# Kernel tuning notes

Measured on AMD Instinct MI355X. Metric: run time of the kernel, lower is better.

## Reference

```python
import jax, jax.numpy as jnp
import numpy as np

# structural constants (from dg config / init_kwargs)
B = 8192      # batch (L=1)
N = 64        # number of columns
C = 16        # one-hot width per column
D = N * C     # 1024
NUM = 32      # first NUM columns are numeric (use info['range'])
NCAUSAL = 16  # causal_cols = range(16)
K = 8         # info['range'][i] is [C, K]
HS = 1024
HP = 1024
TAU = 0.7
SMOOTH = 0.1  # kwargs['smoothing']


def setup_inputs() -> dict:
    key = jax.random.key(0)
    ks = jax.random.split(key, 20)
    s = 0.02
    inp = {
        'x': jax.random.uniform(ks[0], (B, D), dtype=jnp.float32),
        'truth_x': jax.random.normal(ks[1], (B, N), dtype=jnp.float32),
        # selector: Linear(D,HS) -> ReLU -> Linear(HS,N) -> Sigmoid
        'sel_w1': jax.random.normal(ks[2], (D, HS)) * s,
        'sel_b1': jnp.zeros((HS,), jnp.float32),
        'sel_w2': jax.random.normal(ks[3], (HS, N)) * s,
        'sel_b2': jnp.zeros((N,), jnp.float32),
        # perturber: D->HP->HP->HP->D with ReLU between
        'pw1': jax.random.normal(ks[4], (D, HP)) * s,
        'pb1': jnp.zeros((HP,), jnp.float32),
        'pw2': jax.random.normal(ks[5], (HP, HP)) * s,
        'pb2': jnp.zeros((HP,), jnp.float32),
        'pw3': jax.random.normal(ks[6], (HP, HP)) * s,
        'pb3': jnp.zeros((HP,), jnp.float32),
        'pw4': jax.random.normal(ks[7], (HP, D)) * s,
        'pb4': jnp.zeros((D,), jnp.float32),
        # dg.info['range'][i] for numeric columns: [NUM, C, K]
        'ranges': jax.random.normal(ks[8], (NUM, C, K), dtype=jnp.float32),
        # pre-drawn noise (training branch)
        'unif_a': jax.random.uniform(ks[9], (B, N), minval=1e-6, maxval=1.0 - 1e-6),
        'unif_b': jax.random.uniform(ks[10], (B, N), minval=1e-6, maxval=1.0 - 1e-6),
        'gumbel': jax.random.gumbel(ks[11], (B, N, C), dtype=jnp.float32),
    }
    return inp


def reference(x, truth_x, sel_w1, sel_b1, sel_w2, sel_b2,
              pw1, pb1, pw2, pb2, pw3, pb3, pw4, pb4,
              ranges, unif_a, unif_b, gumbel):
    # selector -> P in (0,1), shape [B, N]
    P = jax.nn.sigmoid(jax.nn.relu(x @ sel_w1 + sel_b1) @ sel_w2 + sel_b2)
    # relaxed Bernoulli (Sample_Bernoulli, training branch)
    ga = -jnp.log(-jnp.log(unif_a))
    gb = -jnp.log(-jnp.log(unif_b))
    no_logits = P * jnp.exp(ga) / TAU
    de_logits = no_logits + (1.0 - P) * jnp.exp(gb) / TAU
    probs = no_logits / de_logits                       # [B, N]
    # perturber MLP -> W, shape [B, D]
    h = jax.nn.relu(x @ pw1 + pb1)
    h = jax.nn.relu(h @ pw2 + pb2)
    h = jax.nn.relu(h @ pw3 + pb3)
    W = h @ pw4 + pb4
    # per-column blocks
    xr = x.reshape(B, N, C)
    logits = W.reshape(B, N, C)
    # data-dependent causal masking for causal columns
    curr = jnp.argmax(xr, axis=-1)                      # [B, N]
    causal = (jnp.arange(N) < NCAUSAL)[None, :, None]   # [1, N, 1]
    below = jnp.arange(C)[None, None, :] < curr[:, :, None]
    mask = jnp.where(causal & below, -100.0, jnp.where(causal, 1.0, 0.0))
    logits = logits + mask
    # label smoothing then Gumbel-softmax (soft), per Sample_Categorical
    pr = jax.nn.softmax(logits, axis=-1)
    pr = (1.0 - SMOOTH) * pr + SMOOTH / C
    logits = jnp.log(pr)
    y = jax.nn.softmax((logits + gumbel) / TAU, axis=-1)  # [B, N, C]
    # numeric columns: map categorical sample through range table, mix with truth
    xt_num = jnp.einsum('bnc,nck->bnk', y[:, :NUM], ranges).mean(axis=-1)  # [B, NUM]
    p_num = probs[:, :NUM]
    out_num = p_num * xt_num + (1.0 - p_num) * truth_x[:, :NUM]           # [B, NUM]
    # categorical columns: mix relaxed sample with original one-hot block
    p_cat = probs[:, NUM:, None]
    out_cat = p_cat * y[:, NUM:] + (1.0 - p_cat) * xr[:, NUM:]            # [B, N-NUM, C]
    xcf = jnp.concatenate([out_num, out_cat.reshape(B, (N - NUM) * C)], axis=1)
    return truth_x, xcf, P, W
```

## Files before the change

### kernel.cpp

```cpp
#include <hip/hip_runtime.h>
#include <hip/hip_bf16.h>
#include <cstdint>

#define B_DIM 8192
#define N_DIM 64
#define C_DIM 16
#define D_DIM 1024
#define NUM 32
#define NCAUSAL 16
#define K_RANGES 8
#define HS 1024
#define HP 1024
#define TAU 0.7f
#define SMOOTH 0.1f

typedef __bf16 bf16x8 __attribute__((ext_vector_type(8)));
typedef float f32x16 __attribute__((ext_vector_type(16)));

typedef const __attribute__((address_space(1))) uint32_t* gas_ptr;
typedef __attribute__((address_space(3))) uint32_t* las_ptr;

__device__ __forceinline__ void gld_lds16(const void* g, void* l) {
    __builtin_amdgcn_global_load_lds((gas_ptr)(uintptr_t)g,
                                     (las_ptr)(uint32_t)(uintptr_t)l,
                                     16, 0, 0);
}

__device__ __forceinline__ int swz(int r) { return (r & 3) ^ ((r >> 2) & 3); }

template <int ACT>
__device__ __forceinline__ void gemm_body8(
    const ushort* __restrict__ Ag, const ushort* __restrict__ Bg,
    const float* __restrict__ bias,
    float* __restrict__ Cf, __hip_bfloat16* __restrict__ Cb,
    int lda, int Nout, int ldC, int K, long m0, long n0,
    uint4 (*As)[512], uint4 (*Bs)[512])
{
    const int tid  = threadIdx.x;
    const int wave = tid >> 6;
    const int ln31 = tid & 31, blk = (tid >> 5) & 1;
    const int wr = wave >> 2, wc = wave & 3;

    const int row = tid >> 2;
    const int ch  = (tid & 3) ^ swz(row);
    const ushort* aSrc = Ag + (m0 + row) * (long)lda + ch * 8;
    const ushort* bSrc = Bg + (n0 + row) * (long)K   + ch * 8;
    const int ldsOff = wave << 6;

    f32x16 acc[2];
    acc[0] = (f32x16)(0.0f);
    acc[1] = (f32x16)(0.0f);

#define ISSUE_STAGE8(buf, kt)                                                  \
    {                                                                          \
        gld_lds16(aSrc + (kt), &As[buf][ldsOff]);                              \
        gld_lds16(bSrc + (kt), &Bs[buf][ldsOff]);                              \
    }

    ISSUE_STAGE8(0, 0);
    int cur = 0;
    for (int kt = 0; kt < K; kt += 32) {
        __syncthreads();
        if (kt + 32 < K) ISSUE_STAGE8(cur ^ 1, kt + 32);

        bf16x8 af[2][2], bfr[2];
#pragma unroll
        for (int ks = 0; ks < 2; ++ks) {
            int c = ks * 2 + blk;
#pragma unroll
            for (int mi = 0; mi < 2; ++mi) {
                int r = wr * 64 + mi * 32 + ln31;
                af[ks][mi] = __builtin_bit_cast(bf16x8, As[cur][r * 4 + (c ^ swz(r))]);
            }
            int n = wc * 32 + ln31;
            bfr[ks] = __builtin_bit_cast(bf16x8, Bs[cur][n * 4 + (c ^ swz(n))]);
        }
#pragma unroll
        for (int ks = 0; ks < 2; ++ks)
#pragma unroll
            for (int mi = 0; mi < 2; ++mi)
                acc[mi] = __builtin_amdgcn_mfma_f32_32x32x16_bf16(
                    af[ks][mi], bfr[ks], acc[mi], 0, 0, 0);
        cur ^= 1;
    }
#undef ISSUE_STAGE8

    long col = n0 + wc * 32 + ln31;
    if (col < Nout) {
        float bs = bias ? bias[col] : 0.0f;
#pragma unroll
        for (int mi = 0; mi < 2; ++mi) {
#pragma unroll
            for (int reg = 0; reg < 16; ++reg) {
                long r2 = m0 + wr * 64 + mi * 32 + (reg & 3) + 8 * (reg >> 2) + 4 * blk;
                float v = acc[mi][reg] + bs;
                if (ACT == 1) {
                    v = fmaxf(v, 0.0f);
                    Cb[r2 * (long)ldC + col] = __float2bfloat16(v);
                } else if (ACT == 2) {
                    v = 1.0f / (1.0f + __expf(-v));
                    Cf[r2 * (long)ldC + col] = v;
                } else {
                    Cf[r2 * (long)ldC + col] = v;
                }
            }
        }
    }
}

template <int ACT>
__global__ __launch_bounds__(512, 4) void gemm8(
    const __hip_bfloat16* __restrict__ A, const __hip_bfloat16* __restrict__ Bt,
    const float* __restrict__ bias,
    float* __restrict__ Cf, __hip_bfloat16* __restrict__ Cb,
    int lda, int Nout, int ldC, int K)
{
    __shared__ uint4 As[2][512];
    __shared__ uint4 Bs[2][512];
    gemm_body8<ACT>((const ushort*)A, (const ushort*)Bt, bias, Cf, Cb,
                    lda, Nout, ldC, K,
                    (long)blockIdx.y * 128, (long)blockIdx.x * 128, As, Bs);
}

__global__ __launch_bounds__(512, 4) void gemm8_fused23(
    const __hip_bfloat16* __restrict__ act1,
    const __hip_bfloat16* __restrict__ p2t, const float* __restrict__ pb2,
    __hip_bfloat16* __restrict__ actB,
    const __hip_bfloat16* __restrict__ w2t, const float* __restrict__ sel_b2,
    float* __restrict__ outP)
{
    __shared__ uint4 As[2][512];
    __shared__ uint4 Bs[2][512];
    long m0 = (long)blockIdx.y * 128;
    if (blockIdx.x < 8) {
        gemm_body8<1>((const ushort*)(act1 + 1024), (const ushort*)p2t, pb2,
                      nullptr, actB, 2048, 1024, 1024, 1024,
                      m0, (long)blockIdx.x * 128, As, Bs);
    } else {
        gemm_body8<2>((const ushort*)act1, (const ushort*)w2t, sel_b2,
                      outP, nullptr, 2048, 64, 64, 1024,
                      m0, 0, As, Bs);
    }
}

struct PrepArgs {
    const float* src[6];
    __hip_bfloat16* dst[6];
    int Nsrc[6];
    int Npad[6];
    const float* ranges; float* rmean;
    const float* b1; const float* b2; float* bcat;
    const float* x; __hip_bfloat16* xbf;
};

__global__ void prep_kernel(PrepArgs a)
{
    int z = blockIdx.z;
    int tx = threadIdx.x, ty = threadIdx.y;
    int t = ty * 32 + tx;
    if (z == 7) {
        int bid = blockIdx.y * 32 + blockIdx.x;
        const float4* s4 = (const float4*)a.x;
        for (int i = bid * 256 + t; i < B_DIM * D_DIM / 4; i += 1024 * 256) {
            float4 v = s4[i];
            __hip_bfloat16* d = a.xbf + (size_t)i * 4;
            d[0] = __float2bfloat16(v.x);
            d[1] = __float2bfloat16(v.y);
            d[2] = __float2bfloat16(v.z);
            d[3] = __float2bfloat16(v.w);
        }
        return;
    }
    if (z == 6) {
        if (blockIdx.x || blockIdx.y) return;
        for (int j = t; j < NUM * C_DIM; j += 256) {
            float s = 0.0f;
#pragma unroll
            for (int k = 0; k < K_RANGES; ++k) s += a.ranges[j * K_RANGES + k];
            a.rmean[j] = s * (1.0f / K_RANGES);
        }
        for (int j = t; j < 1024; j += 256) {
            a.bcat[j]        = a.b1[j];
            a.bcat[1024 + j] = a.b2[j];
        }
        return;
    }
    const int Nsrc = a.Nsrc[z], Npad = a.Npad[z];
    int n0 = blockIdx.x * 32, k0 = blockIdx.y * 32;
    if (n0 >= Npad) return;
    const float* src = a.src[z];
    __hip_bfloat16* dst = a.dst[z];
    __shared__ float tile[32][33];
#pragma unroll
    for (int i = 0; i < 32; i += 8) {
        int k = k0 + ty + i, n = n0 + tx;
        tile[ty + i][tx] = (n < Nsrc) ? src[(size_t)k * Nsrc + n] : 0.0f;
    }
    __syncthreads();
#pragma unroll
    for (int i = 0; i < 32; i += 8) {
        int n = n0 + ty + i, k = k0 + tx;
        dst[(size_t)n * D_DIM + k] = __float2bfloat16(tile[tx][ty + i]);
    }
}

__global__ void finalize_kernel(
    const float* __restrict__ x, const float* __restrict__ truth,
    const float* __restrict__ ua, const float* __restrict__ ub,
    const float* __restrict__ gum, const float* __restrict__ rmean,
    const float* __restrict__ P, const float* __restrict__ W,
    float* __restrict__ out_truth, float* __restrict__ out_xcf)
{
    int idx = blockIdx.x * 256 + threadIdx.x;
    if (idx >= B_DIM * N_DIM) return;
    int b = idx >> 6, n = idx & 63;

    float tx = truth[idx];
    out_truth[idx] = tx;

    float p  = P[idx];
    float ea = -1.0f / logf(ua[idx]);
    float eb = -1.0f / logf(ub[idx]);
    float no = p * ea;
    float probs = no / (no + (1.0f - p) * eb);

    const float* Wrow = W + (size_t)idx * 16;
    const float* grow = gum + (size_t)idx * 16;
    float lo[16], g[16], xv[16];
#pragma unroll
    for (int c = 0; c < 16; c += 4) {
        float4 v = *(const float4*)(Wrow + c);
        lo[c] = v.x; lo[c + 1] = v.y; lo[c + 2] = v.z; lo[c + 3] = v.w;
        float4 gv = *(const float4*)(grow + c);
        g[c] = gv.x; g[c + 1] = gv.y; g[c + 2] = gv.z; g[c + 3] = gv.w;
    }

    bool needx = (n < NCAUSAL) || (n >= NUM);
    if (needx) {
        const float* xrow = x + (size_t)idx * 16;
#pragma unroll
        for (int c = 0; c < 16; c += 4) {
            float4 v = *(const float4*)(xrow + c);
            xv[c] = v.x; xv[c + 1] = v.y; xv[c + 2] = v.z; xv[c + 3] = v.w;
        }
    }

    if (n < NCAUSAL) {
        int curr = 0; float best = xv[0];
#pragma unroll
        for (int c = 1; c < 16; ++c)
            if (xv[c] > best) { best = xv[c]; curr = c; }
#pragma unroll
        for (int c = 0; c < 16; ++c) lo[c] += (c < curr) ? -100.0f : 1.0f;
    }

    float mx = lo[0];
#pragma unroll
    for (int c = 1; c < 16; ++c) mx = fmaxf(mx, lo[c]);
    float s = 0.0f, pr[16];
#pragma unroll
    for (int c = 0; c < 16; ++c) { pr[c] = __expf(lo[c] - mx); s += pr[c]; }
    float inv = 1.0f / s;
#pragma unroll
    for (int c = 0; c < 16; ++c)
        pr[c] = (1.0f - SMOOTH) * pr[c] * inv + (SMOOTH / C_DIM);

    float t[16];
    float mx2 = -1e30f;
#pragma unroll
    for (int c = 0; c < 16; ++c) {
        t[c] = (__logf(pr[c]) + g[c]) * (1.0f / TAU);
        mx2 = fmaxf(mx2, t[c]);
    }
    float s2 = 0.0f;
#pragma unroll
    for (int c = 0; c < 16; ++c) { t[c] = __expf(t[c] - mx2); s2 += t[c]; }
    float inv2 = 1.0f / s2;

    if (n < NUM) {
        float xt = 0.0f;
#pragma unroll
        for (int c = 0; c < 16; ++c) xt += t[c] * inv2 * rmean[n * 16 + c];
        out_xcf[(size_t)b * 544 + n] = probs * xt + (1.0f - probs) * tx;
    } else {
        float* o = out_xcf + (size_t)b * 544 + 32 + (size_t)(n - NUM) * 16;
#pragma unroll
        for (int c = 0; c < 16; ++c)
            o[c] = probs * t[c] * inv2 + (1.0f - probs) * xv[c];
    }
}

extern "C" void kernel_launch(void* const* d_in, const int* in_sizes, int n_in,
                              void* d_out, int out_size, void* d_ws, size_t ws_size,
                              hipStream_t stream)
{
    const float* x      = (const float*)d_in[0];
    const float* truth  = (const float*)d_in[1];
    const float* sel_w1 = (const float*)d_in[2];
    const float* sel_b1 = (const float*)d_in[3];
    const float* sel_w2 = (const float*)d_in[4];
    const float* sel_b2 = (const float*)d_in[5];
    const float* pw1    = (const float*)d_in[6];
    const float* pb1    = (const float*)d_in[7];
    const float* pw2    = (const float*)d_in[8];
    const float* pb2    = (const float*)d_in[9];
    const float* pw3    = (const float*)d_in[10];
    const float* pb3    = (const float*)d_in[11];
    const float* pw4    = (const float*)d_in[12];
    const float* pb4    = (const float*)d_in[13];
    const float* ranges = (const float*)d_in[14];
    const float* ua     = (const float*)d_in[15];
    const float* ub     = (const float*)d_in[16];
    const float* gum    = (const float*)d_in[17];

    float* out       = (float*)d_out;
    float* out_truth = out;
    float* out_xcf   = out + 524288;
    float* out_P     = out + 4980736;
    float* out_W     = out + 5505024;

    char* w = (char*)d_ws;
    size_t off = 0;
    __hip_bfloat16* A0   = (__hip_bfloat16*)(w + off); off += (size_t)B_DIM * D_DIM * 2;
    __hip_bfloat16* act1 = (__hip_bfloat16*)(w + off); off += (size_t)B_DIM * 2048 * 2;
    __hip_bfloat16* actB = (__hip_bfloat16*)(w + off); off += (size_t)B_DIM * HP * 2;
    __hip_bfloat16* actC = (__hip_bfloat16*)(w + off); off += (size_t)B_DIM * HP * 2;
    __hip_bfloat16* Wcat = (__hip_bfloat16*)(w + off); off += (size_t)2048 * D_DIM * 2;
    __hip_bfloat16* w2t  = (__hip_bfloat16*)(w + off); off += (size_t)128 * HS * 2;
    __hip_bfloat16* p2t  = (__hip_bfloat16*)(w + off); off += (size_t)HP * HP * 2;
    __hip_bfloat16* p3t  = (__hip_bfloat16*)(w + off); off += (size_t)HP * HP * 2;
    __hip_bfloat16* p4t  = (__hip_bfloat16*)(w + off); off += (size_t)D_DIM * HP * 2;
    float* rmean         = (float*)(w + off);          off += 512 * 4;
    float* bcat          = (float*)(w + off);          off += 2048 * 4;
    if (ws_size < off) return;

    PrepArgs pa;
    pa.src[0] = sel_w1; pa.dst[0] = Wcat;               pa.Nsrc[0] = HS;    pa.Npad[0] = 1024;
    pa.src[1] = pw1;    pa.dst[1] = Wcat + 1024 * 1024; pa.Nsrc[1] = HP;    pa.Npad[1] = 1024;
    pa.src[2] = sel_w2; pa.dst[2] = w2t;                pa.Nsrc[2] = N_DIM; pa.Npad[2] = 128;
    pa.src[3] = pw2;    pa.dst[3] = p2t;                pa.Nsrc[3] = HP;    pa.Npad[3] = 1024;
    pa.src[4] = pw3;    pa.dst[4] = p3t;                pa.Nsrc[4] = HP;    pa.Npad[4] = 1024;
    pa.src[5] = pw4;    pa.dst[5] = p4t;                pa.Nsrc[5] = D_DIM; pa.Npad[5] = 1024;
    pa.ranges = ranges; pa.rmean = rmean;
    pa.b1 = sel_b1; pa.b2 = pb1; pa.bcat = bcat;
    pa.x = x; pa.xbf = A0;

    prep_kernel<<<dim3(32, 32, 8), dim3(32, 8), 0, stream>>>(pa);

    gemm8<1><<<dim3(16, 64), 512, 0, stream>>>(A0, Wcat, bcat, nullptr, act1,
                                               D_DIM, 2048, 2048, D_DIM);
    gemm8_fused23<<<dim3(9, 64), 512, 0, stream>>>(act1, p2t, pb2, actB, w2t,
                                                   sel_b2, out_P);
    gemm8<1><<<dim3(8, 64), 512, 0, stream>>>(actB, p3t, pb3, nullptr, actC,
                                              HP, HP, HP, HP);
    gemm8<0><<<dim3(8, 64), 512, 0, stream>>>(actC, p4t, pb4, out_W, nullptr,
                                              HP, D_DIM, D_DIM, HP);

    finalize_kernel<<<(B_DIM * N_DIM + 255) / 256, 256, 0, stream>>>(
        x, truth, ua, ub, gum, rmean, out_P, out_W, out_truth, out_xcf);
}
```

Before: 306.3 us.

## Triple-buffer GEMM LDS pipeline and remap workgroups across XCDs

Moves the bf16 MFMA GEMM mainloop from double to triple buffering. It uses explicit vmcnt waits so two K-tiles of global-to-LDS loads are in flight while one is consumed, which is meant to hide more memory latency. It also adds an XCD-aware remap of workgroup indices so consecutive tiles land on the same XCD and share L2. The cost is 50% more LDS per block, which could limit occupancy. The remap assumes the workgroup count is divisible by 8.

```diff
diff --git a/kernel.cpp b/kernel.cpp
--- a/kernel.cpp
+++ b/kernel.cpp
@@ -57,11 +57,23 @@
         gld_lds16(bSrc + (kt), &Bs[buf][ldsOff]);                              \
     }
 
+    const int nt = K >> 5;
     ISSUE_STAGE8(0, 0);
-    int cur = 0;
-    for (int kt = 0; kt < K; kt += 32) {
-        __syncthreads();
-        if (kt + 32 < K) ISSUE_STAGE8(cur ^ 1, kt + 32);
+    ISSUE_STAGE8(1, 32);
+
+    int rb = 0;
+    for (int t = 0; t < nt; ++t) {
+        if (t < nt - 1) {
+            asm volatile("s_waitcnt vmcnt(2)" ::: "memory");
+        } else {
+            asm volatile("s_waitcnt vmcnt(0)" ::: "memory");
+        }
+        __builtin_amdgcn_s_barrier();
+
+        if (t + 2 < nt) {
+            int sb = rb + 2; if (sb >= 3) sb -= 3;
+            ISSUE_STAGE8(sb, (t + 2) * 32);
+        }
 
         bf16x8 af[2][2], bfr[2];
 #pragma unroll
@@ -70,10 +82,10 @@
 #pragma unroll
             for (int mi = 0; mi < 2; ++mi) {
                 int r = wr * 64 + mi * 32 + ln31;
-                af[ks][mi] = __builtin_bit_cast(bf16x8, As[cur][r * 4 + (c ^ swz(r))]);
+                af[ks][mi] = __builtin_bit_cast(bf16x8, As[rb][r * 4 + (c ^ swz(r))]);
             }
             int n = wc * 32 + ln31;
-            bfr[ks] = __builtin_bit_cast(bf16x8, Bs[cur][n * 4 + (c ^ swz(n))]);
+            bfr[ks] = __builtin_bit_cast(bf16x8, Bs[rb][n * 4 + (c ^ swz(n))]);
         }
 #pragma unroll
         for (int ks = 0; ks < 2; ++ks)
@@ -81,7 +93,8 @@
             for (int mi = 0; mi < 2; ++mi)
                 acc[mi] = __builtin_amdgcn_mfma_f32_32x32x16_bf16(
                     af[ks][mi], bfr[ks], acc[mi], 0, 0, 0);
-        cur ^= 1;
+
+        rb = (rb == 2) ? 0 : rb + 1;
     }
 #undef ISSUE_STAGE8
 
@@ -108,6 +121,17 @@
     }
 }
 
+__device__ __forceinline__ void xcd_remap(int& bx, int& by)
+{
+    int gx  = gridDim.x;
+    int nwg = gx * gridDim.y;
+    int lin = by * gx + bx;
+    int cpx = nwg >> 3;
+    int sw  = (lin & 7) * cpx + (lin >> 3);
+    by = sw / gx;
+    bx = sw - by * gx;
+}
+
 template <int ACT>
 __global__ __launch_bounds__(512, 4) void gemm8(
     const __hip_bfloat16* __restrict__ A, const __hip_bfloat16* __restrict__ Bt,
@@ -115,11 +139,13 @@
     float* __restrict__ Cf, __hip_bfloat16* __restrict__ Cb,
     int lda, int Nout, int ldC, int K)
 {
-    __shared__ uint4 As[2][512];
-    __shared__ uint4 Bs[2][512];
+    __shared__ uint4 As[3][512];
+    __shared__ uint4 Bs[3][512];
+    int bx = blockIdx.x, by = blockIdx.y;
+    xcd_remap(bx, by);
     gemm_body8<ACT>((const ushort*)A, (const ushort*)Bt, bias, Cf, Cb,
                     lda, Nout, ldC, K,
-                    (long)blockIdx.y * 128, (long)blockIdx.x * 128, As, Bs);
+                    (long)by * 128, (long)bx * 128, As, Bs);
 }
 
 __global__ __launch_bounds__(512, 4) void gemm8_fused23(
@@ -129,13 +155,15 @@
     const __hip_bfloat16* __restrict__ w2t, const float* __restrict__ sel_b2,
     float* __restrict__ outP)
 {
-    __shared__ uint4 As[2][512];
-    __shared__ uint4 Bs[2][512];
-    long m0 = (long)blockIdx.y * 128;
-    if (blockIdx.x < 8) {
+    __shared__ uint4 As[3][512];
+    __shared__ uint4 Bs[3][512];
+    int bx = blockIdx.x, by = blockIdx.y;
+    xcd_remap(bx, by);
+    long m0 = (long)by * 128;
+    if (bx < 8) {
         gemm_body8<1>((const ushort*)(act1 + 1024), (const ushort*)p2t, pb2,
                       nullptr, actB, 2048, 1024, 1024, 1024,
-                      m0, (long)blockIdx.x * 128, As, Bs);
+                      m0, (long)bx * 128, As, Bs);
     } else {
         gemm_body8<2>((const ushort*)act1, (const ushort*)w2t, sel_b2,
                       outP, nullptr, 2048, 64, 64, 1024,
```

Result: faster. 293.7 us (-4.1%).

## Use 128x64 GEMM tiles with XCD-aware block remap for perturber layers

Applied to the files above, without the earlier changes.

Adds a 256-thread GEMM body that computes 128x64 output tiles. Layers 2-4 and the fused selector-output kernel now use it, doubling the block count for better occupancy and load balance across CUs. The fused kernel's N=64 sigmoid path now loads only 64 weight columns instead of a padded 128-column tile. All GEMMs remap block indices so that neighbouring tiles land on the same XCD, to improve L2 reuse. Launch bounds are raised to 8 blocks, which may squeeze register budgets, and the smaller tiles cut per-block data reuse.

```diff
diff --git a/kernel.cpp b/kernel.cpp
--- a/kernel.cpp
+++ b/kernel.cpp
@@ -27,6 +27,17 @@
 }
 
 __device__ __forceinline__ int swz(int r) { return (r & 3) ^ ((r >> 2) & 3); }
+
+__device__ __forceinline__ void xcd_remap(int& bx, int& by)
+{
+    int gx  = gridDim.x;
+    int nwg = gx * gridDim.y;
+    int lin = by * gx + bx;
+    int cpx = nwg >> 3;
+    int sw  = (lin & 7) * cpx + (lin >> 3);
+    by = sw / gx;
+    bx = sw - by * gx;
+}
 
 template <int ACT>
 __device__ __forceinline__ void gemm_body8(
@@ -109,7 +120,91 @@
 }
 
 template <int ACT>
-__global__ __launch_bounds__(512, 4) void gemm8(
+__device__ __forceinline__ void gemm_body4(
+    const ushort* __restrict__ Ag, const ushort* __restrict__ Bg,
+    const float* __restrict__ bias,
+    float* __restrict__ Cf, __hip_bfloat16* __restrict__ Cb,
+    int lda, int Nout, int ldC, int K, long m0, long n0,
+    uint4 (*As)[512], uint4 (*Bs)[256])
+{
+    const int tid  = threadIdx.x;
+    const int wave = tid >> 6;
+    const int ln31 = tid & 31, blk = (tid >> 5) & 1;
+    const int wr = (wave >> 1) & 1, wc = wave & 1;
+
+    const int r0  = tid >> 2;
+    const int ch0 = (tid & 3) ^ swz(r0);
+    const int r1  = 64 + r0;
+    const int ch1 = (tid & 3) ^ swz(r1);
+    const ushort* aSrc0 = Ag + (m0 + r0) * (long)lda + ch0 * 8;
+    const ushort* aSrc1 = Ag + (m0 + r1) * (long)lda + ch1 * 8;
+    const ushort* bSrc  = Bg + (n0 + r0) * (long)K   + ch0 * 8;
+    const int ldsOff = wave << 6;
+
+    f32x16 acc[2];
+    acc[0] = (f32x16)(0.0f);
+    acc[1] = (f32x16)(0.0f);
+
+#define ISSUE_STAGE4(buf, kt)                                                  \
+    {                                                                          \
+        gld_lds16(aSrc0 + (kt), &As[buf][ldsOff]);                             \
+        gld_lds16(aSrc1 + (kt), &As[buf][256 + ldsOff]);                       \
+        gld_lds16(bSrc  + (kt), &Bs[buf][ldsOff]);                             \
+    }
+
+    ISSUE_STAGE4(0, 0);
+    int cur = 0;
+    for (int kt = 0; kt < K; kt += 32) {
+        __syncthreads();
+        if (kt + 32 < K) ISSUE_STAGE4(cur ^ 1, kt + 32);
+
+        bf16x8 af[2][2], bfr[2];
+#pragma unroll
+        for (int ks = 0; ks < 2; ++ks) {
+            int c = ks * 2 + blk;
+#pragma unroll
+            for (int mi = 0; mi < 2; ++mi) {
+                int r = wr * 64 + mi * 32 + ln31;
+                af[ks][mi] = __builtin_bit_cast(bf16x8, As[cur][r * 4 + (c ^ swz(r))]);
+            }
+            int n = wc * 32 + ln31;
+            bfr[ks] = __builtin_bit_cast(bf16x8, Bs[cur][n * 4 + (c ^ swz(n))]);
+        }
+#pragma unroll
+        for (int ks = 0; ks < 2; ++ks)
+#pragma unroll
+            for (int mi = 0; mi < 2; ++mi)
+                acc[mi] = __builtin_amdgcn_mfma_f32_32x32x16_bf16(
+                    af[ks][mi], bfr[ks], acc[mi], 0, 0, 0);
+        cur ^= 1;
+    }
+#undef ISSUE_STAGE4
+
+    long col = n0 + wc * 32 + ln31;
+    if (col < Nout) {
+        float bs = bias ? bias[col] : 0.0f;
+#pragma unroll
+        for (int mi = 0; mi < 2; ++mi) {
+#pragma unroll
+            for (int reg = 0; reg < 16; ++reg) {
+                long r2 = m0 + wr * 64 + mi * 32 + (reg & 3) + 8 * (reg >> 2) + 4 * blk;
+                float v = acc[mi][reg] + bs;
+                if (ACT == 1) {
+                    v = fmaxf(v, 0.0f);
+                    Cb[r2 * (long)ldC + col] = __float2bfloat16(v);
+                } else if (ACT == 2) {
+                    v = 1.0f / (1.0f + __expf(-v));
+                    Cf[r2 * (long)ldC + col] = v;
+                } else {
+                    Cf[r2 * (long)ldC + col] = v;
+                }
+            }
+        }
+    }
+}
+
+template <int ACT>
+__global__ __launch_bounds__(512, 8) void gemm8(
     const __hip_bfloat16* __restrict__ A, const __hip_bfloat16* __restrict__ Bt,
     const float* __restrict__ bias,
     float* __restrict__ Cf, __hip_bfloat16* __restrict__ Cb,
@@ -117,12 +212,30 @@
 {
     __shared__ uint4 As[2][512];
     __shared__ uint4 Bs[2][512];
+    int bx = blockIdx.x, by = blockIdx.y;
+    xcd_remap(bx, by);
     gemm_body8<ACT>((const ushort*)A, (const ushort*)Bt, bias, Cf, Cb,
                     lda, Nout, ldC, K,
-                    (long)blockIdx.y * 128, (long)blockIdx.x * 128, As, Bs);
-}
-
-__global__ __launch_bounds__(512, 4) void gemm8_fused23(
+                    (long)by * 128, (long)bx * 128, As, Bs);
+}
+
+template <int ACT>
+__global__ __launch_bounds__(256, 8) void gemm4(
+    const __hip_bfloat16* __restrict__ A, const __hip_bfloat16* __restrict__ Bt,
+    const float* __restrict__ bias,
+    float* __restrict__ Cf, __hip_bfloat16* __restrict__ Cb,
+    int lda, int Nout, int ldC, int K)
+{
+    __shared__ uint4 As[2][512];
+    __shared__ uint4 Bs[2][256];
+    int bx = blockIdx.x, by = blockIdx.y;
+    xcd_remap(bx, by);
+    gemm_body4<ACT>((const ushort*)A, (const ushort*)Bt, bias, Cf, Cb,
+                    lda, Nout, ldC, K,
+                    (long)by * 128, (long)bx * 64, As, Bs);
+}
+
+__global__ __launch_bounds__(256, 8) void gemm4_fused23(
     const __hip_bfloat16* __restrict__ act1,
     const __hip_bfloat16* __restrict__ p2t, const float* __restrict__ pb2,
     __hip_bfloat16* __restrict__ actB,
@@ -130,14 +243,16 @@
     float* __restrict__ outP)
 {
     __shared__ uint4 As[2][512];
-    __shared__ uint4 Bs[2][512];
-    long m0 = (long)blockIdx.y * 128;
-    if (blockIdx.x < 8) {
-        gemm_body8<1>((const ushort*)(act1 + 1024), (const ushort*)p2t, pb2,
+    __shared__ uint4 Bs[2][256];
+    int bx = blockIdx.x, by = blockIdx.y;
+    xcd_remap(bx, by);
+    long m0 = (long)by * 128;
+    if (bx < 16) {
+        gemm_body4<1>((const ushort*)(act1 + 1024), (const ushort*)p2t, pb2,
                       nullptr, actB, 2048, 1024, 1024, 1024,
-                      m0, (long)blockIdx.x * 128, As, Bs);
+                      m0, (long)bx * 64, As, Bs);
     } else {
-        gemm_body8<2>((const ushort*)act1, (const ushort*)w2t, sel_b2,
+        gemm_body4<2>((const ushort*)act1, (const ushort*)w2t, sel_b2,
                       outP, nullptr, 2048, 64, 64, 1024,
                       m0, 0, As, Bs);
     }
@@ -349,12 +464,12 @@
 
     gemm8<1><<<dim3(16, 64), 512, 0, stream>>>(A0, Wcat, bcat, nullptr, act1,
                                                D_DIM, 2048, 2048, D_DIM);
-    gemm8_fused23<<<dim3(9, 64), 512, 0, stream>>>(act1, p2t, pb2, actB, w2t,
-                                                   sel_b2, out_P);
-    gemm8<1><<<dim3(8, 64), 512, 0, stream>>>(actB, p3t, pb3, nullptr, actC,
-                                              HP, HP, HP, HP);
-    gemm8<0><<<dim3(8, 64), 512, 0, stream>>>(actC, p4t, pb4, out_W, nullptr,
-                                              HP, D_DIM, D_DIM, HP);
+    gemm4_fused23<<<dim3(17, 64), 256, 0, stream>>>(act1, p2t, pb2, actB, w2t,
+                                                    sel_b2, out_P);
+    gemm4<1><<<dim3(16, 64), 256, 0, stream>>>(actB, p3t, pb3, nullptr, actC,
+                                               HP, HP, HP, HP);
+    gemm4<0><<<dim3(16, 64), 256, 0, stream>>>(actC, p4t, pb4, out_W, nullptr,
+                                               HP, D_DIM, D_DIM, HP);
 
     finalize_kernel<<<(B_DIM * N_DIM + 255) / 256, 256, 0, stream>>>(
         x, truth, ua, ub, gum, rmean, out_P, out_W, out_truth, out_xcf);
```

Result: slower. 314.7 us (+2.7%).
